# Kernel optimization log

Measured on AMD Instinct MI355X. Metric: run time of the kernel, lower is better.

## Reference

```python
import jax, jax.numpy as jnp
import numpy as np

N = 50000          # num nodes
E = 800000         # num edges (avg degree 16)
C_IN = 64          # input channels
TOWERS = 4
F_IN = C_IN // TOWERS       # 16 (divide_input=True)
OUT = 128
F_OUT = OUT // TOWERS       # 32
NUM_AGG = 4                 # mean, std, max, min
NUM_SC = 3                  # identity, amplification, attenuation
AVG_LOG_DEG = float(np.log(17.0))  # deg histogram: all nodes degree 16 -> log(16+1)


def setup_inputs() -> dict:
    key = jax.random.key(0)
    ks = jax.random.split(key, 10)
    nodes = jax.random.normal(ks[0], (N, C_IN), dtype=jnp.float32)
    senders = jax.random.randint(ks[1], (E,), 0, N)
    receivers = jax.random.randint(ks[2], (E,), 0, N)
    # per-tower pre-MLP: Linear(2*F_IN -> F_IN), pre_layers=1 (no activation)
    pre_w = jax.random.normal(ks[3], (TOWERS, 2 * F_IN, F_IN), dtype=jnp.float32) / np.sqrt(2 * F_IN)
    pre_b = jnp.zeros((TOWERS, F_IN), dtype=jnp.float32)
    # per-tower post-MLP: Linear(F_IN + F_IN*12 -> F_OUT), post_layers=1
    post_in = F_IN + F_IN * NUM_AGG * NUM_SC  # 208
    post_w = jax.random.normal(ks[4], (TOWERS, post_in, F_OUT), dtype=jnp.float32) / np.sqrt(post_in)
    post_b = jnp.zeros((TOWERS, F_OUT), dtype=jnp.float32)
    # final linear: TOWERS*F_OUT -> OUT
    lin_w = jax.random.normal(ks[5], (TOWERS * F_OUT, OUT), dtype=jnp.float32) / np.sqrt(TOWERS * F_OUT)
    lin_b = jnp.zeros((OUT,), dtype=jnp.float32)
    return {"nodes": nodes, "senders": senders, "receivers": receivers,
            "pre_w": pre_w, "pre_b": pre_b, "post_w": post_w, "post_b": post_b,
            "lin_w": lin_w, "lin_b": lin_b}


def reference(nodes, senders, receivers, pre_w, pre_b, post_w, post_b, lin_w, lin_b):
    # divide_input=True: split channels across towers -> [N, T, F_IN]
    x = nodes.reshape(N, TOWERS, F_IN)
    x_i = x[senders]                                  # [E, T, F_IN]
    x_j = x[receivers]                                # [E, T, F_IN]
    h = jnp.concatenate([x_i, x_j], axis=-1)          # [E, T, 2*F_IN]
    # per-tower pre-MLP (single linear), vectorized over towers
    msg = jnp.einsum('etf,tfo->eto', h, pre_w) + pre_b  # [E, T, F_IN]

    # degree-scaled multi-aggregator segment reduce over receivers
    count = jax.ops.segment_sum(jnp.ones((E,), dtype=msg.dtype), receivers, num_segments=N)  # [N]
    d = jnp.clip(count, 1.0, None)
    inv_d = (1.0 / d)[:, None, None]
    mean = jax.ops.segment_sum(msg, receivers, num_segments=N) * inv_d           # [N,T,F]
    mean_sq = jax.ops.segment_sum(msg * msg, receivers, num_segments=N) * inv_d
    std = jnp.sqrt(jax.nn.relu(mean_sq - mean * mean) + 1e-5)
    has_nb = (count > 0)[:, None, None]
    mx = jax.ops.segment_max(msg, receivers, num_segments=N)
    mx = jnp.where(has_nb, mx, 0.0)
    mn = -jax.ops.segment_max(-msg, receivers, num_segments=N)
    mn = jnp.where(has_nb, mn, 0.0)
    agg = jnp.concatenate([mean, std, mx, mn], axis=-1)  # [N, T, 4*F_IN]

    # scalers: identity, amplification, attenuation (degree clamped to >= 1)
    log_d = jnp.log(d + 1.0)[:, None, None]
    amp = log_d / AVG_LOG_DEG
    att = AVG_LOG_DEG / log_d
    scaled = jnp.concatenate([agg, agg * amp, agg * att], axis=-1)  # [N, T, 12*F_IN]

    out = jnp.concatenate([x, scaled], axis=-1)                     # [N, T, 13*F_IN]
    outs = jnp.einsum('ntf,tfo->nto', out, post_w) + post_b         # [N, T, F_OUT]
    flat = outs.reshape(N, TOWERS * F_OUT)                          # [N, 128]
    return flat @ lin_w + lin_b                                     # [N, OUT]
```

## Files before the change

kernel.cpp:

```cpp
#include <hip/hip_runtime.h>

#define AVG_LOG_DEG 2.8332133440562162f
#define CAP 64
#define CSTRIDE 16

typedef __attribute__((ext_vector_type(8))) short short8;
typedef __attribute__((ext_vector_type(4))) float f32x4;

static __device__ __forceinline__ float bl(unsigned u) { return __uint_as_float(u << 16); }
static __device__ __forceinline__ float bh(unsigned u) { return __uint_as_float(u & 0xffff0000u); }
static __device__ __forceinline__ unsigned short f2b(float f) {
    unsigned u = __float_as_uint(f);
    return (unsigned short)((u + 0x7fffu + ((u >> 16) & 1u)) >> 16);
}
static __device__ __forceinline__ unsigned pk(unsigned short lo, unsigned short hi) {
    return (unsigned)lo | ((unsigned)hi << 16);
}


__global__ __launch_bounds__(256) void k_setup(
    const float* __restrict__ nodes, const float* __restrict__ pre_w,
    const float* __restrict__ pre_b,
    const float* __restrict__ post_w, const float* __restrict__ lin_w,
    const int* __restrict__ send, const int* __restrict__ recv,
    unsigned short* __restrict__ Yh, float* __restrict__ H,
    unsigned short* __restrict__ postT, unsigned short* __restrict__ linT,
    int* __restrict__ cursor, int* __restrict__ wcntG, int2* __restrict__ bktArr,
    int n, int A, int nZ, int nbZ, int e)
{
    __shared__ int2 stage[2048];
    __shared__ int wcnt[4][8], btot[8], pref[9];

    int b = blockIdx.x;
    int tid = threadIdx.x;
    if (b < A) {
        int lane = tid & 63;
        int wid = tid >> 6;
        int t = lane >> 4, f = lane & 15;
        float w0[16], w1[16];
        #pragma unroll
        for (int k = 0; k < 16; ++k) {
            w0[k] = pre_w[(t * 32 + k) * 16 + f];
            w1[k] = pre_w[(t * 32 + 16 + k) * 16 + f];
        }
        float hb = pre_b[t * 16 + f];
        int nbase = b * 16 + wid * 4;
        #pragma unroll
        for (int jj = 0; jj < 4; ++jj) {
            int node = nbase + jj;
            if (node >= n) break;
            const float4* xp = reinterpret_cast<const float4*>(nodes + (size_t)node * 64 + t * 16);
            float4 x0 = xp[0], x1 = xp[1], x2 = xp[2], x3 = xp[3];
            float xs[16] = {x0.x, x0.y, x0.z, x0.w, x1.x, x1.y, x1.z, x1.w,
                            x2.x, x2.y, x2.z, x2.w, x3.x, x3.y, x3.z, x3.w};
            float y = 0.f;
            float h = hb;
            #pragma unroll
            for (int k = 0; k < 16; ++k) {
                y = fmaf(xs[k], w0[k], y);
                h = fmaf(xs[k], w1[k], h);
            }
            Yh[(size_t)node * 64 + lane] = f2b(y);
            H[(size_t)node * 64 + lane] = h;
        }
    } else if (b < A + 176) {
        int i = (b - A) * 256 + tid;
        if (i < 28672) {
            int t = i / (32 * 224);
            int r = i % (32 * 224);
            int nn = r / 224;
            int k = r % 224;
            float wv;
            if (k < 192)      wv = post_w[((size_t)t * 208 + 16 + k) * 32 + nn];
            else if (k < 208) wv = post_w[((size_t)t * 208 + (k - 192)) * 32 + nn];
            else              wv = 0.f;
            postT[i] = f2b(wv);
        }
        int j = i - 28672;
        if (j >= 0 && j < 16384) {
            int nn = j >> 7, k = j & 127;
            linT[j] = f2b(lin_w[k * 128 + nn]);
        }
    } else if (b < A + 176 + nbZ) {
        int i = (b - A - 176) * 1024 + tid * 4;
        if (i < nZ) {
            int4 z; z.x = z.y = z.z = z.w = 0;
            *reinterpret_cast<int4*>(cursor + i) = z;
        }
    } else {
        int bb = b - A - 176 - nbZ;
        int lane = tid & 63, wid = tid >> 6;
        int base = bb * 2048 + wid * 512 + lane;

        int rv[8], sv[8], rk[8];
        unsigned long long lt = (1ULL << lane) - 1ULL;
        unsigned long long runLo = 0, runHi = 0;

        #pragma unroll
        for (int q = 0; q < 8; ++q) {
            int idx = base + q * 64;
            bool valid = idx < e;
            rv[q] = valid ? recv[idx] : 0;
            sv[q] = valid ? send[idx] : 0;
            int bkb = rv[q] & 7;
            unsigned long long m0 = __ballot(bkb & 1);
            unsigned long long m1 = __ballot(bkb & 2);
            unsigned long long m2 = __ballot(bkb & 4);
            unsigned long long mv = __ballot(valid);
            unsigned long long mo = ((bkb & 1) ? m0 : ~m0) & ((bkb & 2) ? m1 : ~m1)
                                  & ((bkb & 4) ? m2 : ~m2) & mv;
            unsigned long long sel = (bkb & 4) ? runHi : runLo;
            int runb = (int)((sel >> ((bkb & 3) * 16)) & 0xffffULL);
            rk[q] = runb + __popcll(mo & lt);
            unsigned long long addLo = 0, addHi = 0;
            #pragma unroll
            for (int k = 0; k < 4; ++k) {
                unsigned long long mkl = ((k & 1) ? m0 : ~m0) & ((k & 2) ? m1 : ~m1) & ~m2 & mv;
                unsigned long long mkh = ((k & 1) ? m0 : ~m0) & ((k & 2) ? m1 : ~m1) &  m2 & mv;
                addLo |= (unsigned long long)__popcll(mkl) << (k * 16);
                addHi |= (unsigned long long)__popcll(mkh) << (k * 16);
            }
            runLo += addLo; runHi += addHi;
            if (!valid) rk[q] = -1;
        }
        if (lane < 8) {
            unsigned long long sel = (lane & 4) ? runHi : runLo;
            wcnt[wid][lane] = (int)((sel >> ((lane & 3) * 16)) & 0xffffULL);
        }
        __syncthreads();
        if (tid < 8) {
            int c0 = wcnt[0][tid], c1 = wcnt[1][tid], c2 = wcnt[2][tid], c3 = wcnt[3][tid];
            wcnt[0][tid] = 0;
            wcnt[1][tid] = c0;
            wcnt[2][tid] = c0 + c1;
            wcnt[3][tid] = c0 + c1 + c2;
            int bt = c0 + c1 + c2 + c3;
            btot[tid] = bt;
            wcntG[bb * 8 + tid] = bt;
        }
        __syncthreads();
        if (tid == 0) {
            int acc = 0;
            #pragma unroll
            for (int k = 0; k < 8; ++k) { pref[k] = acc; acc += btot[k]; }
            pref[8] = acc;
        }
        __syncthreads();
        #pragma unroll
        for (int q = 0; q < 8; ++q) {
            if (rk[q] >= 0) {
                int bkb = rv[q] & 7;
                int pos = pref[bkb] + wcnt[wid][bkb] + rk[q];
                int2 ed; ed.x = rv[q]; ed.y = sv[q];
                stage[pos] = ed;
            }
        }
        __syncthreads();
        int tot = pref[8];
        for (int i = tid; i < tot; i += 256) {
            int k = 0;
            #pragma unroll
            for (int j = 1; j < 8; ++j) k += (i >= pref[j]);
            int g = i - pref[k];
            if (g < 2048)
                bktArr[((size_t)bb * 8 + k) * 2048 + g] = stage[i];
        }
    }
}


__global__ __launch_bounds__(256) void k_scatter2(
    const int* __restrict__ wcntG, const int2* __restrict__ bktArr,
    int* __restrict__ cursor, int* __restrict__ slots, int nseg)
{
    int bkt = blockIdx.x & 7;
    int grp = blockIdx.x >> 3;
    for (int s = grp; s < nseg; s += 256) {
        int cnt = min(wcntG[s * 8 + bkt], 2048);
        const int2* ba = bktArr + ((size_t)s * 8 + bkt) * 2048;
        for (int i = threadIdx.x; i < cnt; i += 256) {
            int2 ed = ba[i];
            int p = atomicAdd(&cursor[(size_t)ed.x * CSTRIDE], 1);
            if (p < CAP) slots[(size_t)ed.x * CAP + p] = ed.y;
        }
    }
}


__global__ __launch_bounds__(256) void k_agg(
    const int* __restrict__ cursor,
    const int* __restrict__ slots,
    const unsigned short* __restrict__ Yh,
    const float* __restrict__ H,
    unsigned short* __restrict__ aggh, int n)
{
    int lane = threadIdx.x & 63;
    int node = blockIdx.x * 4 + (threadIdx.x >> 6);
    if (node >= n) return;
    int t = lane >> 4, f = lane & 15;

    int idxv = slots[(size_t)node * CAP + lane];
    float hjw = H[(size_t)node * 64 + lane];
    int d = min(cursor[(size_t)node * CSTRIDE], CAP);
    const unsigned short* Yl = Yh + lane;

    float s = 0.f, s2 = 0.f, mx = -INFINITY, mn = INFINITY;
    int e = 0;
    for (; e + 16 <= d; e += 16) {
        unsigned v[16];
        #pragma unroll
        for (int q = 0; q < 16; ++q) {
            int si = __builtin_amdgcn_readlane(idxv, e + q);
            v[q] = Yl[(size_t)si * 64];
        }
        #pragma unroll
        for (int q = 0; q < 16; ++q) {
            float m = __uint_as_float(v[q] << 16) + hjw;
            s += m;
            s2 = fmaf(m, m, s2);
            mx = fmaxf(mx, m);
            mn = fminf(mn, m);
        }
    }
    int rem = d - e;
    if (rem > 0) {
        unsigned v[16];
        #pragma unroll
        for (int q = 0; q < 16; ++q) {
            int si = __builtin_amdgcn_readlane(idxv, min(e + q, d - 1));
            v[q] = Yl[(size_t)si * 64];
        }
        #pragma unroll
        for (int q = 0; q < 16; ++q) {
            if (q < rem) {
                float m = __uint_as_float(v[q] << 16) + hjw;
                s += m;
                s2 = fmaf(m, m, s2);
                mx = fmaxf(mx, m);
                mn = fminf(mn, m);
            }
        }
    }

    float dc = fmaxf((float)d, 1.f);
    float inv = 1.f / dc;
    float mean = s * inv;
    float var = fmaf(-mean, mean, s2 * inv);
    float sd = sqrtf(fmaxf(var, 0.f) + 1e-5f);
    if (d == 0) { mx = 0.f; mn = 0.f; }

    unsigned short* ag = aggh + (size_t)node * 256 + t * 64 + f;
    ag[0]  = f2b(mean);
    ag[16] = f2b(sd);
    ag[32] = f2b(mx);
    ag[48] = f2b(mn);
}


__global__ __launch_bounds__(256, 3) void k_post(
    const float* __restrict__ nodes,
    const unsigned short* __restrict__ aggh,
    const int* __restrict__ deg,
    const unsigned short* __restrict__ postT,
    const unsigned short* __restrict__ linT,
    const float* __restrict__ post_b,
    const float* __restrict__ lin_b,
    float* __restrict__ out, int n)
{
    __shared__ unsigned short sV[32 * 256];
    __shared__ unsigned short sFlat[32 * 128];
    __shared__ float sAmp[32], sAtt[32];

    int tid = threadIdx.x;
    int n0 = blockIdx.x * 32;

    if (tid < 32) {
        int g = min(n0 + tid, n - 1);
        float dc = fmaxf((float)min(deg[(size_t)g * CSTRIDE], CAP), 1.f);
        float ld = logf(dc + 1.f);
        sAmp[tid] = ld * (1.f / AVG_LOG_DEG);
        sAtt[tid] = AVG_LOG_DEG / ld;
    }

    int w = tid >> 6, lane = tid & 63;
    int quad = lane >> 4, mr = lane & 15;
    int mstrip = w & 1, nhalf = w >> 1;
    int nn = tid >> 3, j8 = tid & 7;
    int sw = nn & 7;
    int gn = min(n0 + nn, n - 1);
    int rsw = mr & 7;

    uint4 pa4[4];
    #pragma unroll
    for (int t = 0; t < 4; ++t)
        pa4[t] = *reinterpret_cast<const uint4*>(aggh + (size_t)gn * 256 + t * 64 + j8 * 8);

    uint4 xw4[4];
    #pragma unroll
    for (int t = 0; t < 4; ++t) { xw4[t].x = 0; xw4[t].y = 0; xw4[t].z = 0; xw4[t].w = 0; }
    if (j8 < 2) {
        #pragma unroll
        for (int t = 0; t < 4; ++t) {
            const float4* xp = reinterpret_cast<const float4*>(nodes + (size_t)gn * 64 + t * 16 + j8 * 8);
            float4 xa = xp[0], xb = xp[1];
            xw4[t].x = pk(f2b(xa.x), f2b(xa.y)); xw4[t].y = pk(f2b(xa.z), f2b(xa.w));
            xw4[t].z = pk(f2b(xb.x), f2b(xb.y)); xw4[t].w = pk(f2b(xb.z), f2b(xb.w));
        }
    }

    const unsigned short* bbase = postT + (size_t)(nhalf * 16 + mr) * 224 + quad * 8;
    short8 bA[7], bB[7];
    #pragma unroll
    for (int kk = 0; kk < 7; ++kk) bA[kk] = *reinterpret_cast<const short8*>(bbase + kk * 32);
    #pragma unroll
    for (int kk = 0; kk < 7; ++kk) bB[kk] = *reinterpret_cast<const short8*>(bbase + 32 * 224 + kk * 32);

    __syncthreads();
    float ampv = sAmp[nn], attv = sAtt[nn];

    #pragma unroll
    for (int t = 0; t < 4; ++t) {
        {
            unsigned short* row = &sV[nn * 256];
            uint4 a = pa4[t];
            *reinterpret_cast<uint4*>(row + (j8 ^ sw) * 8) = a;
            unsigned uu[4] = {a.x, a.y, a.z, a.w};
            unsigned short pa[8], pb[8];
            #pragma unroll
            for (int q = 0; q < 4; ++q) {
                float lo = bl(uu[q]), hi = bh(uu[q]);
                pa[2*q]   = f2b(lo * ampv); pa[2*q+1] = f2b(hi * ampv);
                pb[2*q]   = f2b(lo * attv); pb[2*q+1] = f2b(hi * attv);
            }
            uint4 wa, wb;
            wa.x = pk(pa[0], pa[1]); wa.y = pk(pa[2], pa[3]);
            wa.z = pk(pa[4], pa[5]); wa.w = pk(pa[6], pa[7]);
            wb.x = pk(pb[0], pb[1]); wb.y = pk(pb[2], pb[3]);
            wb.z = pk(pb[4], pb[5]); wb.w = pk(pb[6], pb[7]);
            *reinterpret_cast<uint4*>(row + (8  + (j8 ^ sw)) * 8) = wa;
            *reinterpret_cast<uint4*>(row + (16 + (j8 ^ sw)) * 8) = wb;
            *reinterpret_cast<uint4*>(row + (24 + (j8 ^ sw)) * 8) = xw4[t];
        }
        __syncthreads();

        f32x4 acc = {0.f, 0.f, 0.f, 0.f};
        const unsigned short* av0 = &sV[(mstrip * 16 + mr) * 256];
        #pragma unroll
        for (int kk = 0; kk < 7; ++kk) {
            int c = kk * 4 + quad;
            int pc = (c & ~7) | ((c & 7) ^ rsw);
            short8 avv = *reinterpret_cast<const short8*>(av0 + pc * 8);
            if (t & 1) acc = __builtin_amdgcn_mfma_f32_16x16x32_bf16(avv, bB[kk], acc, 0, 0, 0);
            else       acc = __builtin_amdgcn_mfma_f32_16x16x32_bf16(avv, bA[kk], acc, 0, 0, 0);
        }

        if (t == 0) {
            #pragma unroll
            for (int kk = 0; kk < 7; ++kk)
                bA[kk] = *reinterpret_cast<const short8*>(bbase + 2 * 32 * 224 + kk * 32);
        } else if (t == 1) {
            #pragma unroll
            for (int kk = 0; kk < 7; ++kk)
                bB[kk] = *reinterpret_cast<const short8*>(bbase + 3 * 32 * 224 + kk * 32);
        }

        int col = t * 32 + nhalf * 16 + mr;
        float pbv = post_b[col];
        int cc = col >> 3, co = col & 7;
        #pragma unroll
        for (int i = 0; i < 4; ++i) {
            int rowf = mstrip * 16 + quad * 4 + i;
            int pc = (cc & ~7) | ((cc & 7) ^ (rowf & 7));
            sFlat[rowf * 128 + pc * 8 + co] = f2b(acc[i] + pbv);
        }
        __syncthreads();
    }

    f32x4 facc[4];
    #pragma unroll
    for (int nt = 0; nt < 4; ++nt) { facc[nt].x = 0.f; facc[nt].y = 0.f; facc[nt].z = 0.f; facc[nt].w = 0.f; }

    const unsigned short* af0 = &sFlat[(mstrip * 16 + mr) * 128];
    #pragma unroll
    for (int kk = 0; kk < 4; ++kk) {
        int c = kk * 4 + quad;
        int pc = (c & ~7) | ((c & 7) ^ rsw);
        short8 avv = *reinterpret_cast<const short8*>(af0 + pc * 8);
        #pragma unroll
        for (int nt = 0; nt < 4; ++nt) {
            short8 bv = *reinterpret_cast<const short8*>(
                linT + (size_t)(nhalf * 64 + nt * 16 + mr) * 128 + kk * 32 + quad * 8);
            facc[nt] = __builtin_amdgcn_mfma_f32_16x16x32_bf16(avv, bv, facc[nt], 0, 0, 0);
        }
    }

    #pragma unroll
    for (int nt = 0; nt < 4; ++nt) {
        int col = nhalf * 64 + nt * 16 + mr;
        float lb = lin_b[col];
        #pragma unroll
        for (int i = 0; i < 4; ++i) {
            int node = n0 + mstrip * 16 + quad * 4 + i;
            if (node < n) out[(size_t)node * 128 + col] = facc[nt][i] + lb;
        }
    }
}

extern "C" void kernel_launch(void* const* d_in, const int* in_sizes, int n_in,
                              void* d_out, int out_size, void* d_ws, size_t ws_size,
                              hipStream_t stream)
{
    const float* nodes  = (const float*)d_in[0];
    const int*   send   = (const int*)d_in[1];
    const int*   recv   = (const int*)d_in[2];
    const float* pre_w  = (const float*)d_in[3];
    const float* pre_b  = (const float*)d_in[4];
    const float* post_w = (const float*)d_in[5];
    const float* post_b = (const float*)d_in[6];
    const float* lin_w  = (const float*)d_in[7];
    const float* lin_b  = (const float*)d_in[8];
    float* out = (float*)d_out;

    int N = in_sizes[0] / 64;
    int E = in_sizes[1];
    int Npad = (N + 255) & ~255;
    int nbBin = (E + 2047) / 2048;

    int* cursor = (int*)d_ws;
    int* wcntG  = cursor + (size_t)Npad * CSTRIDE;
    int2* bktArr = (int2*)(wcntG + (size_t)nbBin * 8);
    int* slots  = (int*)(bktArr + (size_t)nbBin * 8 * 2048);
    unsigned short* Yh = (unsigned short*)(slots + (size_t)Npad * CAP);
    float* H = (float*)(Yh + (size_t)Npad * 64);
    unsigned short* aggh  = (unsigned short*)(H + (size_t)Npad * 64);
    unsigned short* postT = aggh + (size_t)Npad * 256;
    unsigned short* linT  = postT + 28672;

    int nZ = Npad * CSTRIDE;
    int nbZ = (nZ + 1023) / 1024;
    int A = (N + 15) / 16;

    k_setup   <<<A + 176 + nbZ + nbBin, 256, 0, stream>>>(
        nodes, pre_w, pre_b, post_w, lin_w, send, recv,
        Yh, H, postT, linT, cursor, wcntG, bktArr, N, A, nZ, nbZ, E);
    k_scatter2<<<2048, 256, 0, stream>>>(wcntG, bktArr, cursor, slots, nbBin);
    k_agg     <<<(N + 3) / 4, 256, 0, stream>>>(cursor, slots, Yh, H, aggh, N);
    k_post    <<<(N + 31) / 32, 256, 0, stream>>>(nodes, aggh, cursor, postT, linT,
                                                  post_b, lin_b, out, N);
}
```

Baseline: 200.0 us.

## Fuse aggregation kernel into post-MLP kernel via shared-memory aggregates

Moves the per-node multi-aggregator gather and reduction into the post kernel. Each wave reduces 8 nodes and writes the bf16 aggregates and the degree scalers to LDS, so the aggh global buffer and one kernel launch go away. The trade-off is 16KB more LDS per block, which may cut occupancy under launch_bounds(256,3). The latency-bound gather now runs serially across 8 nodes per wave before the MFMA phase, with fewer independent waves left to hide gather latency.

Result: slower. 223.1 us (+11.6%).

```diff
diff --git a/kernel.cpp b/kernel.cpp
--- a/kernel.cpp
+++ b/kernel.cpp
@@ -187,102 +187,97 @@
 }
 
 
-__global__ __launch_bounds__(256) void k_agg(
+__global__ __launch_bounds__(256, 3) void k_post(
+    const float* __restrict__ nodes,
     const int* __restrict__ cursor,
     const int* __restrict__ slots,
     const unsigned short* __restrict__ Yh,
     const float* __restrict__ H,
-    unsigned short* __restrict__ aggh, int n)
-{
-    int lane = threadIdx.x & 63;
-    int node = blockIdx.x * 4 + (threadIdx.x >> 6);
-    if (node >= n) return;
-    int t = lane >> 4, f = lane & 15;
-
-    int idxv = slots[(size_t)node * CAP + lane];
-    float hjw = H[(size_t)node * 64 + lane];
-    int d = min(cursor[(size_t)node * CSTRIDE], CAP);
-    const unsigned short* Yl = Yh + lane;
-
-    float s = 0.f, s2 = 0.f, mx = -INFINITY, mn = INFINITY;
-    int e = 0;
-    for (; e + 16 <= d; e += 16) {
-        unsigned v[16];
-        #pragma unroll
-        for (int q = 0; q < 16; ++q) {
-            int si = __builtin_amdgcn_readlane(idxv, e + q);
-            v[q] = Yl[(size_t)si * 64];
-        }
-        #pragma unroll
-        for (int q = 0; q < 16; ++q) {
-            float m = __uint_as_float(v[q] << 16) + hjw;
-            s += m;
-            s2 = fmaf(m, m, s2);
-            mx = fmaxf(mx, m);
-            mn = fminf(mn, m);
-        }
-    }
-    int rem = d - e;
-    if (rem > 0) {
-        unsigned v[16];
-        #pragma unroll
-        for (int q = 0; q < 16; ++q) {
-            int si = __builtin_amdgcn_readlane(idxv, min(e + q, d - 1));
-            v[q] = Yl[(size_t)si * 64];
-        }
-        #pragma unroll
-        for (int q = 0; q < 16; ++q) {
-            if (q < rem) {
-                float m = __uint_as_float(v[q] << 16) + hjw;
-                s += m;
-                s2 = fmaf(m, m, s2);
-                mx = fmaxf(mx, m);
-                mn = fminf(mn, m);
-            }
-        }
-    }
-
-    float dc = fmaxf((float)d, 1.f);
-    float inv = 1.f / dc;
-    float mean = s * inv;
-    float var = fmaf(-mean, mean, s2 * inv);
-    float sd = sqrtf(fmaxf(var, 0.f) + 1e-5f);
-    if (d == 0) { mx = 0.f; mn = 0.f; }
-
-    unsigned short* ag = aggh + (size_t)node * 256 + t * 64 + f;
-    ag[0]  = f2b(mean);
-    ag[16] = f2b(sd);
-    ag[32] = f2b(mx);
-    ag[48] = f2b(mn);
-}
-
-
-__global__ __launch_bounds__(256, 3) void k_post(
-    const float* __restrict__ nodes,
-    const unsigned short* __restrict__ aggh,
-    const int* __restrict__ deg,
     const unsigned short* __restrict__ postT,
     const unsigned short* __restrict__ linT,
     const float* __restrict__ post_b,
     const float* __restrict__ lin_b,
     float* __restrict__ out, int n)
 {
+    __shared__ unsigned short sAgg[32 * 256];
     __shared__ unsigned short sV[32 * 256];
     __shared__ unsigned short sFlat[32 * 128];
     __shared__ float sAmp[32], sAtt[32];
 
     int tid = threadIdx.x;
     int n0 = blockIdx.x * 32;
-
-    if (tid < 32) {
-        int g = min(n0 + tid, n - 1);
-        float dc = fmaxf((float)min(deg[(size_t)g * CSTRIDE], CAP), 1.f);
-        float ld = logf(dc + 1.f);
-        sAmp[tid] = ld * (1.f / AVG_LOG_DEG);
-        sAtt[tid] = AVG_LOG_DEG / ld;
-    }
-
-    int w = tid >> 6, lane = tid & 63;
+    int lane = tid & 63;
+    int w = tid >> 6;
+
+    {
+        int t = lane >> 4, f = lane & 15;
+        const unsigned short* Yl = Yh + lane;
+        for (int j = 0; j < 8; ++j) {
+            int nl = w * 8 + j;
+            int node = min(n0 + nl, n - 1);
+            int idxv = slots[(size_t)node * CAP + lane];
+            float hjw = H[(size_t)node * 64 + lane];
+            int d = min(cursor[(size_t)node * CSTRIDE], CAP);
+
+            float s = 0.f, s2 = 0.f, mx = -INFINITY, mn = INFINITY;
+            int e = 0;
+            for (; e + 16 <= d; e += 16) {
+                unsigned v[16];
+                #pragma unroll
+                for (int q = 0; q < 16; ++q) {
+                    int si = __builtin_amdgcn_readlane(idxv, e + q);
+                    v[q] = Yl[(size_t)si * 64];
+                }
+                #pragma unroll
+                for (int q = 0; q < 16; ++q) {
+                    float m = __uint_as_float(v[q] << 16) + hjw;
+                    s += m;
+                    s2 = fmaf(m, m, s2);
+                    mx = fmaxf(mx, m);
+                    mn = fminf(mn, m);
+                }
+            }
+            int rem = d - e;
+            if (rem > 0) {
+                unsigned v[16];
+                #pragma unroll
+                for (int q = 0; q < 16; ++q) {
+                    int si = __builtin_amdgcn_readlane(idxv, min(e + q, d - 1));
+                    v[q] = Yl[(size_t)si * 64];
+                }
+                #pragma unroll
+                for (int q = 0; q < 16; ++q) {
+                    if (q < rem) {
+                        float m = __uint_as_float(v[q] << 16) + hjw;
+                        s += m;
+                        s2 = fmaf(m, m, s2);
+                        mx = fmaxf(mx, m);
+                        mn = fminf(mn, m);
+                    }
+                }
+            }
+
+            float dc = fmaxf((float)d, 1.f);
+            float inv = 1.f / dc;
+            float mean = s * inv;
+            float var = fmaf(-mean, mean, s2 * inv);
+            float sd = sqrtf(fmaxf(var, 0.f) + 1e-5f);
+            if (d == 0) { mx = 0.f; mn = 0.f; }
+
+            unsigned short* ag = &sAgg[nl * 256 + t * 64 + f];
+            ag[0]  = f2b(mean);
+            ag[16] = f2b(sd);
+            ag[32] = f2b(mx);
+            ag[48] = f2b(mn);
+            if (lane == 0) {
+                float ld = logf(dc + 1.f);
+                sAmp[nl] = ld * (1.f / AVG_LOG_DEG);
+                sAtt[nl] = AVG_LOG_DEG / ld;
+            }
+        }
+    }
+    __syncthreads();
+
     int quad = lane >> 4, mr = lane & 15;
     int mstrip = w & 1, nhalf = w >> 1;
     int nn = tid >> 3, j8 = tid & 7;
@@ -293,7 +288,7 @@
     uint4 pa4[4];
     #pragma unroll
     for (int t = 0; t < 4; ++t)
-        pa4[t] = *reinterpret_cast<const uint4*>(aggh + (size_t)gn * 256 + t * 64 + j8 * 8);
+        pa4[t] = *reinterpret_cast<const uint4*>(&sAgg[nn * 256 + t * 64 + j8 * 8]);
 
     uint4 xw4[4];
     #pragma unroll
@@ -432,8 +427,7 @@
     int* slots  = (int*)(bktArr + (size_t)nbBin * 8 * 2048);
     unsigned short* Yh = (unsigned short*)(slots + (size_t)Npad * CAP);
     float* H = (float*)(Yh + (size_t)Npad * 64);
-    unsigned short* aggh  = (unsigned short*)(H + (size_t)Npad * 64);
-    unsigned short* postT = aggh + (size_t)Npad * 256;
+    unsigned short* postT = (unsigned short*)(H + (size_t)Npad * 64);
     unsigned short* linT  = postT + 28672;
 
     int nZ = Npad * CSTRIDE;
@@ -444,7 +438,6 @@
         nodes, pre_w, pre_b, post_w, lin_w, send, recv,
         Yh, H, postT, linT, cursor, wcntG, bktArr, N, A, nZ, nbZ, E);
     k_scatter2<<<2048, 256, 0, stream>>>(wcntG, bktArr, cursor, slots, nbBin);
-    k_agg     <<<(N + 3) / 4, 256, 0, stream>>>(cursor, slots, Yh, H, aggh, N);
-    k_post    <<<(N + 31) / 32, 256, 0, stream>>>(nodes, aggh, cursor, postT, linT,
-                                                  post_b, lin_b, out, N);
-}
+    k_post    <<<(N + 31) / 32, 256, 0, stream>>>(nodes, cursor, slots, Yh, H,
+                                                  postT, linT, post_b, lin_b, out, N);
+}
```
